# Optimization experiments

Measured on AMD Instinct MI355X. Metric: run time of the kernel, lower is better.

Reference implementation:

```python
import jax, jax.numpy as jnp
import numpy as np

N_NODES = 100000
N_EDGES = 10000
N_PAIRS = 1600000
F = 128


def setup_inputs() -> dict:
    key = jax.random.key(0)
    ks = jax.random.split(key, 7)
    x = jax.random.normal(ks[0], (N_NODES, F), dtype=jnp.float32)
    action = jax.random.uniform(ks[1], (N_NODES, 3), dtype=jnp.float32)
    W_msg = jax.random.normal(ks[2], (F, F), dtype=jnp.float32) * (1.0 / np.sqrt(F))
    W_upd = jax.random.normal(ks[3], (F, F), dtype=jnp.float32) * (1.0 / np.sqrt(F))
    b_upd = jax.random.normal(ks[4], (F,), dtype=jnp.float32) * 0.02
    pair_node = jax.random.randint(ks[5], (N_PAIRS,), 0, N_NODES, dtype=jnp.int32)
    pair_edge = jax.random.randint(ks[6], (N_PAIRS,), 0, N_EDGES, dtype=jnp.int32)
    return {"x": x, "action": action, "W_msg": W_msg, "W_upd": W_upd,
            "b_upd": b_upd, "pair_node": pair_node, "pair_edge": pair_edge}


def _v2v_mean(m, pair_node, pair_edge):
    # v2e: mean of incident node features per hyperedge, then
    # e2v: mean of incident hyperedge features per node.
    ones = jnp.ones((pair_node.shape[0],), dtype=m.dtype)
    edge_deg = jax.ops.segment_sum(ones, pair_edge, num_segments=N_EDGES)
    node_deg = jax.ops.segment_sum(ones, pair_node, num_segments=N_NODES)
    # gather node features to incidence pairs, reduce into edges  [E, F]
    e_feat = jax.ops.segment_sum(m[pair_node], pair_edge, num_segments=N_EDGES)
    e_feat = e_feat / jnp.maximum(edge_deg, 1.0)[:, None]
    # gather edge features back to pairs, reduce into nodes       [N, F]
    v_feat = jax.ops.segment_sum(e_feat[pair_edge], pair_node, num_segments=N_NODES)
    v_feat = v_feat / jnp.maximum(node_deg, 1.0)[:, None]
    return v_feat


def reference(x, action, W_msg, W_upd, b_upd, pair_node, pair_edge):
    send = action[:, 0] + action[:, 2]      # [N]
    receive = action[:, 0] + action[:, 1]   # [N]
    m_ji = x @ W_msg.T                       # lin_message (no bias)
    m_ji = jax.nn.gelu(m_ji, approximate=False)  # dropout=0 (eval)
    m_ji = m_ji * send[:, None]
    m_i = _v2v_mean(m_ji, pair_node, pair_edge)
    m_i = m_i * receive[:, None]
    h_i = jax.nn.gelu(x @ W_upd.T + b_upd + m_i, approximate=False)
    return h_i
```

## Files before the change

### kernel.cpp

```cpp
#include <hip/hip_runtime.h>

#define N_NODESC 100000
#define N_EDGESC 10000
#define N_PAIRSC 1600000
#define FDIM 128

#define NB 200
#define EPB 50
#define NPB 500
#define ECAP2 8704
#define PA_CHUNK 8192
#define PA_NCH ((N_PAIRSC + PA_CHUNK - 1) / PA_CHUNK)
#define MSG_BLKS 782

typedef short bf16x8 __attribute__((ext_vector_type(8)));
typedef float f32x4 __attribute__((ext_vector_type(4)));
typedef float f32x2 __attribute__((ext_vector_type(2)));
typedef int i32x4 __attribute__((ext_vector_type(4)));
typedef unsigned u32x4 __attribute__((ext_vector_type(4)));

__device__ __forceinline__ unsigned short f2b(float f) {
  unsigned u = __float_as_uint(f);
  u += 0x7fffu + ((u >> 16) & 1u);
  return (unsigned short)(u >> 16);
}
__device__ __forceinline__ float b2f(unsigned short b) {
  return __uint_as_float(((unsigned)b) << 16);
}
__device__ __forceinline__ unsigned pack2(float a, float b) {
  return (unsigned)f2b(a) | ((unsigned)f2b(b) << 16);
}
__device__ __forceinline__ float gelu_fast(float z) {
  float z2 = z * z;
  float w = fmaf(0.044715f, z2, 1.0f);
  float e = __expf(1.5957691216f * z * w);
  return z * e * __builtin_amdgcn_rcpf(e + 1.0f);
}
__device__ __forceinline__ bf16x8 ldA(const float* p) {
  float4 u0 = *(const float4*)p;
  float4 u1 = *(const float4*)(p + 4);
  u32x4 w = {pack2(u0.x, u0.y), pack2(u0.z, u0.w), pack2(u1.x, u1.y), pack2(u1.z, u1.w)};
  return __builtin_bit_cast(bf16x8, w);
}

__global__ __launch_bounds__(256) void k_prep(const float* __restrict__ action,
                                              const float* __restrict__ wmsg, const float* __restrict__ wupd,
                                              short* __restrict__ wmsgb, short* __restrict__ wupdb,
                                              float* __restrict__ send, float* __restrict__ recv,
                                              int* __restrict__ gcure, int* __restrict__ gcurn) {
  int i = blockIdx.x * 256 + threadIdx.x;
  if (i < FDIM * FDIM) {
    wmsgb[i] = (short)f2b(wmsg[i]);
    wupdb[i] = (short)f2b(wupd[i]);
  }
  if (i < N_NODESC) {
    float a0 = action[i * 3 + 0], a1 = action[i * 3 + 1], a2 = action[i * 3 + 2];
    send[i] = a0 + a2;
    recv[i] = a0 + a1;
  }
  if (i < NB) {
    gcure[i] = i * ECAP2;
    gcurn[i] = i * ECAP2;
  }
}

__device__ __forceinline__ int wave_incl_scan(int v, int lane) {
#pragma unroll
  for (int d = 1; d < 64; d <<= 1) {
    int n = __shfl_up(v, d, 64);
    if (lane >= d) v += n;
  }
  return v;
}

__global__ __launch_bounds__(256) void k_part_msg(const int* __restrict__ pn, const int* __restrict__ pe,
                                                  int* __restrict__ gcure, int* __restrict__ gcurn,
                                                  unsigned* __restrict__ buckE, unsigned* __restrict__ buckN,
                                                  const float* __restrict__ x, const short* __restrict__ wb,
                                                  const float* __restrict__ send,
                                                  unsigned char* __restrict__ mji8) {
  __shared__ unsigned stage[PA_CHUNK];
  __shared__ int ce[NB], cn[NB];
  int t = threadIdx.x;
  if (blockIdx.x < PA_NCH) {
    for (int i = t; i < NB; i += 256) { ce[i] = 0; cn[i] = 0; }
    __syncthreads();
    long long base = (long long)blockIdx.x * PA_CHUNK;
    for (int q = t; q < PA_CHUNK / 4; q += 256) {
      long long idx = base + (long long)q * 4;
      if (idx >= N_PAIRSC) break;
      i32x4 e4 = __builtin_nontemporal_load((const i32x4*)(pe + idx));
      i32x4 v4 = __builtin_nontemporal_load((const i32x4*)(pn + idx));
#pragma unroll
      for (int j = 0; j < 4; j++) {
        unsigned ee = (unsigned)e4[j], vv = (unsigned)v4[j];
        stage[q + j * (PA_CHUNK / 4)] = (ee << 17) | vv;
        atomicAdd(&ce[ee / EPB], 1);
        atomicAdd(&cn[vv / NPB], 1);
      }
    }
    __syncthreads();
    for (int i = t; i < NB; i += 256) {
      ce[i] = atomicAdd(&gcure[i], ce[i]);
      cn[i] = atomicAdd(&gcurn[i], cn[i]);
    }
    __syncthreads();
    for (int i = t; i < PA_CHUNK; i += 256) {
      int q = i & (PA_CHUNK / 4 - 1), j = i >> 11;
      long long idx = base + (long long)q * 4 + j;
      if (idx >= N_PAIRSC) continue;
      unsigned u = stage[i];
      unsigned ee = u >> 17, vv = u & 0x1FFFF;
      int p1 = atomicAdd(&ce[ee / EPB], 1);
      buckE[p1] = u;
      int p2 = atomicAdd(&cn[vv / NPB], 1);
      buckN[p2] = (vv << 14) | ee;
    }
  } else {
    int gw = ((int)(blockIdx.x - PA_NCH) * 256 + t) >> 6;
    int lane = t & 63;
    if (gw >= N_NODESC / 32) return;
    int rb = gw * 32;
    int lr = lane & 15, lg = lane >> 4;

    bf16x8 A0[4], A1[4];
    const float* xrow0 = x + (size_t)(rb + lr) * FDIM + lg * 8;
    const float* xrow1 = xrow0 + 16 * FDIM;
#pragma unroll
    for (int kk = 0; kk < 4; kk++) {
      A0[kk] = ldA(xrow0 + kk * 32);
      A1[kk] = ldA(xrow1 + kk * 32);
    }
    float sv0[4], sv1[4];
#pragma unroll
    for (int j = 0; j < 4; j++) {
      sv0[j] = send[rb + lg * 4 + j];
      sv1[j] = send[rb + 16 + lg * 4 + j];
    }
#pragma unroll
    for (int c = 0; c < 8; c++) {
      f32x4 acc0 = {0.f, 0.f, 0.f, 0.f}, acc1 = {0.f, 0.f, 0.f, 0.f};
      const short* wrow = wb + (size_t)(16 * c + lr) * FDIM + lg * 8;
#pragma unroll
      for (int kk = 0; kk < 4; kk++) {
        bf16x8 B = *(const bf16x8*)(wrow + kk * 32);
        acc0 = __builtin_amdgcn_mfma_f32_16x16x32_bf16(A0[kk], B, acc0, 0, 0, 0);
        acc1 = __builtin_amdgcn_mfma_f32_16x16x32_bf16(A1[kk], B, acc1, 0, 0, 0);
      }
      int col = 16 * c + lr;
#pragma unroll
      for (int j = 0; j < 4; j++) {
        float m0 = gelu_fast(acc0[j]) * sv0[j];
        float m1 = gelu_fast(acc1[j]) * sv1[j];
        int row0 = rb + lg * 4 + j;
        mji8[(size_t)row0 * FDIM + col] =
            (unsigned char)(__builtin_amdgcn_cvt_pk_fp8_f32(m0, m0, 0, false) & 0xFF);
        mji8[(size_t)(row0 + 16) * FDIM + col] =
            (unsigned char)(__builtin_amdgcn_cvt_pk_fp8_f32(m1, m1, 0, false) & 0xFF);
      }
    }
  }
}

__global__ __launch_bounds__(256) void k_fine_e(const unsigned* __restrict__ buckE,
                                                const int* __restrict__ gcure,
                                                int* __restrict__ ecnt, int* __restrict__ eoff,
                                                int* __restrict__ sn) {
  __shared__ int cnt_s[EPB], cur_s[EPB];
  int b = blockIdx.x, t = threadIdx.x;
  int lo = b * EPB, beg = b * ECAP2, end = gcure[b];
  if (t < EPB) cnt_s[t] = 0;
  __syncthreads();
  for (int i = beg + t; i < end; i += 256)
    atomicAdd(&cnt_s[(int)(buckE[i] >> 17) - lo], 1);
  __syncthreads();
  if (t < 64) {
    int v = (t < EPB) ? cnt_s[t] : 0;
    int inc = wave_incl_scan(v, t);
    if (t < EPB) cur_s[t] = beg + inc - v;
  }
  __syncthreads();
  if (t < EPB) {
    ecnt[lo + t] = cnt_s[t];
    eoff[lo + t] = cur_s[t];
  }
  __syncthreads();
  for (int i = beg + t; i < end; i += 256) {
    unsigned u = buckE[i];
    int key = (int)(u >> 17) - lo;
    int pos = atomicAdd(&cur_s[key], 1);
    sn[pos] = (int)(u & 0x1FFFF);
  }
}

__global__ __launch_bounds__(256) void k_edge_fineN(const unsigned* __restrict__ buckN,
                                                    const int* __restrict__ gcurn,
                                                    int* __restrict__ ncnt, int* __restrict__ noff,
                                                    int* __restrict__ se,
                                                    const unsigned char* __restrict__ mji8,
                                                    const int* __restrict__ sn,
                                                    const int* __restrict__ eoff, const int* __restrict__ ecnt,
                                                    unsigned char* __restrict__ efeat8) {
  __shared__ int cnt_s[NPB], cur_s[NPB];
  int t = threadIdx.x;
  if (blockIdx.x < NB) {
    int b = blockIdx.x;
    int lo = b * NPB, beg = b * ECAP2, end = gcurn[b];
    for (int i = t; i < NPB; i += 256) cnt_s[i] = 0;
    __syncthreads();
    for (int i = beg + t; i < end; i += 256)
      atomicAdd(&cnt_s[(int)(buckN[i] >> 14) - lo], 1);
    __syncthreads();
    if (t < 64) {
      int carry = beg;
#pragma unroll
      for (int base = 0; base < NPB; base += 64) {
        int idx = base + t;
        int v = (idx < NPB) ? cnt_s[idx] : 0;
        int inc = wave_incl_scan(v, t);
        if (idx < NPB) cur_s[idx] = carry + inc - v;
        carry += __shfl(inc, 63, 64);
      }
    }
    __syncthreads();
    for (int i = t; i < NPB; i += 256) {
      ncnt[lo + i] = cnt_s[i];
      noff[lo + i] = cur_s[i];
    }
    __syncthreads();
    for (int i = beg + t; i < end; i += 256) {
      unsigned u = buckN[i];
      int key = (int)(u >> 14) - lo;
      int pos = atomicAdd(&cur_s[key], 1);
      se[pos] = (int)(u & 0x3FFF);
    }
  } else {
    int wave = (int)(blockIdx.x - NB) * 4 + (t >> 6);
    int lane = t & 63;
    int half = lane >> 5, sub2 = (lane >> 4) & 1, c4 = lane & 15;
    int edge = wave * 2 + half;
    if (edge >= N_EDGESC) return;
    int beg = eoff[edge], cnt = ecnt[edge];
    f32x2 a0 = {0.f, 0.f}, a1 = {0.f, 0.f}, a2 = {0.f, 0.f}, a3 = {0.f, 0.f};
#pragma unroll 4
    for (int p = sub2; p < cnt; p += 2) {
      int node = sn[beg + p];
      uint2 u = ((const uint2*)(mji8 + (size_t)node * FDIM))[c4];
      a0 += __builtin_amdgcn_cvt_pk_f32_fp8(u.x, false);
      a1 += __builtin_amdgcn_cvt_pk_f32_fp8(u.x, true);
      a2 += __builtin_amdgcn_cvt_pk_f32_fp8(u.y, false);
      a3 += __builtin_amdgcn_cvt_pk_f32_fp8(u.y, true);
    }
    a0[0] += __shfl_xor(a0[0], 16, 64); a0[1] += __shfl_xor(a0[1], 16, 64);
    a1[0] += __shfl_xor(a1[0], 16, 64); a1[1] += __shfl_xor(a1[1], 16, 64);
    a2[0] += __shfl_xor(a2[0], 16, 64); a2[1] += __shfl_xor(a2[1], 16, 64);
    a3[0] += __shfl_xor(a3[0], 16, 64); a3[1] += __shfl_xor(a3[1], 16, 64);
    if (sub2 == 0) {
      float inv = 1.0f / fmaxf((float)cnt, 1.0f);
      uint2 o;
      o.x = (unsigned)__builtin_amdgcn_cvt_pk_fp8_f32(a0[0] * inv, a0[1] * inv, 0, false);
      o.x = (unsigned)__builtin_amdgcn_cvt_pk_fp8_f32(a1[0] * inv, a1[1] * inv, (int)o.x, true);
      o.y = (unsigned)__builtin_amdgcn_cvt_pk_fp8_f32(a2[0] * inv, a2[1] * inv, 0, false);
      o.y = (unsigned)__builtin_amdgcn_cvt_pk_fp8_f32(a3[0] * inv, a3[1] * inv, (int)o.y, true);
      ((uint2*)(efeat8 + (size_t)edge * FDIM))[c4] = o;
    }
  }
}

__global__ __launch_bounds__(256) void k_node(const unsigned char* __restrict__ efeat8, const int* __restrict__ se,
                                              const int* __restrict__ noff, const int* __restrict__ ncnt,
                                              const float* __restrict__ recv, unsigned char* __restrict__ mi8) {
  int wave = blockIdx.x * 4 + (threadIdx.x >> 6);
  int lane = threadIdx.x & 63;
  int sub = lane >> 4, c4 = lane & 15;
  int node = wave * 4 + sub;
  int beg = noff[node], cnt = ncnt[node];
  f32x2 a0 = {0.f, 0.f}, a1 = {0.f, 0.f}, a2 = {0.f, 0.f}, a3 = {0.f, 0.f};
#pragma unroll 4
  for (int p = 0; p < cnt; p++) {
    int e = se[beg + p];
    uint2 u = ((const uint2*)(efeat8 + (size_t)e * FDIM))[c4];
    a0 += __builtin_amdgcn_cvt_pk_f32_fp8(u.x, false);
    a1 += __builtin_amdgcn_cvt_pk_f32_fp8(u.x, true);
    a2 += __builtin_amdgcn_cvt_pk_f32_fp8(u.y, false);
    a3 += __builtin_amdgcn_cvt_pk_f32_fp8(u.y, true);
  }
  float s = recv[node] / fmaxf((float)cnt, 1.0f);
  uint2 o;
  o.x = (unsigned)__builtin_amdgcn_cvt_pk_fp8_f32(a0[0] * s, a0[1] * s, 0, false);
  o.x = (unsigned)__builtin_amdgcn_cvt_pk_fp8_f32(a1[0] * s, a1[1] * s, (int)o.x, true);
  o.y = (unsigned)__builtin_amdgcn_cvt_pk_fp8_f32(a2[0] * s, a2[1] * s, 0, false);
  o.y = (unsigned)__builtin_amdgcn_cvt_pk_fp8_f32(a3[0] * s, a3[1] * s, (int)o.y, true);
  ((uint2*)(mi8 + (size_t)node * FDIM))[c4] = o;
}

__global__ __launch_bounds__(256) void k_gemm_upd(const float* __restrict__ x, const short* __restrict__ wb,
                                                  const float* __restrict__ bias,
                                                  const unsigned char* __restrict__ mi8,
                                                  float* __restrict__ out) {
  int gw = (blockIdx.x * 256 + threadIdx.x) >> 6;
  int lane = threadIdx.x & 63;
  if (gw >= N_NODESC / 32) return;
  int rb = gw * 32;
  int lr = lane & 15, lg = lane >> 4;

  bf16x8 A0[4], A1[4];
  const float* xrow0 = x + (size_t)(rb + lr) * FDIM + lg * 8;
  const float* xrow1 = xrow0 + 16 * FDIM;
#pragma unroll
  for (int kk = 0; kk < 4; kk++) {
    A0[kk] = ldA(xrow0 + kk * 32);
    A1[kk] = ldA(xrow1 + kk * 32);
  }

#pragma unroll
  for (int c = 0; c < 8; c++) {
    f32x4 acc0 = {0.f, 0.f, 0.f, 0.f}, acc1 = {0.f, 0.f, 0.f, 0.f};
    const short* wrow = wb + (size_t)(16 * c + lr) * FDIM + lg * 8;
#pragma unroll
    for (int kk = 0; kk < 4; kk++) {
      bf16x8 B = *(const bf16x8*)(wrow + kk * 32);
      acc0 = __builtin_amdgcn_mfma_f32_16x16x32_bf16(A0[kk], B, acc0, 0, 0, 0);
      acc1 = __builtin_amdgcn_mfma_f32_16x16x32_bf16(A1[kk], B, acc1, 0, 0, 0);
    }
    int col = 16 * c + lr;
    float bc = bias[col];
#pragma unroll
    for (int j = 0; j < 4; j++) {
      int row0 = rb + lg * 4 + j;
      f32x2 m0 = __builtin_amdgcn_cvt_pk_f32_fp8((unsigned)mi8[(size_t)row0 * FDIM + col], false);
      f32x2 m1 = __builtin_amdgcn_cvt_pk_f32_fp8((unsigned)mi8[(size_t)(row0 + 16) * FDIM + col], false);
      float z0 = acc0[j] + bc + m0[0];
      float z1 = acc1[j] + bc + m1[0];
      __builtin_nontemporal_store(gelu_fast(z0), &out[(size_t)row0 * FDIM + col]);
      __builtin_nontemporal_store(gelu_fast(z1), &out[(size_t)(row0 + 16) * FDIM + col]);
    }
  }
}

extern "C" void kernel_launch(void* const* d_in, const int* in_sizes, int n_in,
                              void* d_out, int out_size, void* d_ws, size_t ws_size,
                              hipStream_t stream) {
  const float* x = (const float*)d_in[0];
  const float* action = (const float*)d_in[1];
  const float* wmsg = (const float*)d_in[2];
  const float* wupd = (const float*)d_in[3];
  const float* bupd = (const float*)d_in[4];
  const int* pn = (const int*)d_in[5];
  const int* pe = (const int*)d_in[6];
  float* out = (float*)d_out;

  char* p = (char*)d_ws;
  auto alloc = [&](size_t bytes) -> char* {
    char* r = p;
    p += (bytes + 255) & ~(size_t)255;
    return r;
  };
  unsigned char* mji8 = (unsigned char*)alloc((size_t)N_NODESC * FDIM);
  unsigned char* mi8 = (unsigned char*)alloc((size_t)N_NODESC * FDIM);
  unsigned char* efeat8 = (unsigned char*)alloc((size_t)N_EDGESC * FDIM);
  unsigned* buckE = (unsigned*)alloc((size_t)NB * ECAP2 * 4);
  unsigned* buckN = (unsigned*)alloc((size_t)NB * ECAP2 * 4);
  int* sn = (int*)alloc((size_t)NB * ECAP2 * 4);
  int* se = (int*)alloc((size_t)NB * ECAP2 * 4);
  short* wmsgb = (short*)alloc(FDIM * FDIM * 2);
  short* wupdb = (short*)alloc(FDIM * FDIM * 2);
  float* send = (float*)alloc(N_NODESC * 4);
  float* recv = (float*)alloc(N_NODESC * 4);
  int* ecnt = (int*)alloc(N_EDGESC * 4);
  int* eoff = (int*)alloc(N_EDGESC * 4);
  int* ncnt = (int*)alloc(N_NODESC * 4);
  int* noff = (int*)alloc(N_NODESC * 4);
  int* gcure = (int*)alloc(NB * 4);
  int* gcurn = (int*)alloc(NB * 4);

  k_prep<<<391, 256, 0, stream>>>(action, wmsg, wupd, wmsgb, wupdb, send, recv, gcure, gcurn);
  k_part_msg<<<PA_NCH + MSG_BLKS, 256, 0, stream>>>(pn, pe, gcure, gcurn, buckE, buckN,
                                                    x, wmsgb, send, mji8);
  k_fine_e<<<NB, 256, 0, stream>>>(buckE, gcure, ecnt, eoff, sn);
  k_edge_fineN<<<NB + 1250, 256, 0, stream>>>(buckN, gcurn, ncnt, noff, se,
                                              mji8, sn, eoff, ecnt, efeat8);
  k_node<<<6250, 256, 0, stream>>>(efeat8, se, noff, ncnt, recv, mi8);
  k_gemm_upd<<<782, 256, 0, stream>>>(x, wupdb, bupd, mi8, out);
}
```

Before: 164.7 us.

## Locally sort partition chunks in LDS so bucket scatters write contiguously

```diff
diff --git a/kernel.cpp b/kernel.cpp
--- a/kernel.cpp
+++ b/kernel.cpp
@@ -9,7 +9,7 @@
 #define EPB 50
 #define NPB 500
 #define ECAP2 8704
-#define PA_CHUNK 8192
+#define PA_CHUNK 6144
 #define PA_NCH ((N_PAIRSC + PA_CHUNK - 1) / PA_CHUNK)
 #define MSG_BLKS 782
 
@@ -80,12 +80,14 @@
                                                   const float* __restrict__ send,
                                                   unsigned char* __restrict__ mji8) {
   __shared__ unsigned stage[PA_CHUNK];
-  __shared__ int ce[NB], cn[NB];
+  __shared__ unsigned ordered[PA_CHUNK];
+  __shared__ int ce[NB], cn[NB], lsE[NB], lsN[NB], curE[NB], curN[NB], gbE[NB], gbN[NB];
   int t = threadIdx.x;
   if (blockIdx.x < PA_NCH) {
     for (int i = t; i < NB; i += 256) { ce[i] = 0; cn[i] = 0; }
     __syncthreads();
     long long base = (long long)blockIdx.x * PA_CHUNK;
+    int nItems = (int)(((long long)N_PAIRSC - base) < PA_CHUNK ? (N_PAIRSC - base) : PA_CHUNK);
     for (int q = t; q < PA_CHUNK / 4; q += 256) {
       long long idx = base + (long long)q * 4;
       if (idx >= N_PAIRSC) break;
@@ -94,27 +96,61 @@
 #pragma unroll
       for (int j = 0; j < 4; j++) {
         unsigned ee = (unsigned)e4[j], vv = (unsigned)v4[j];
-        stage[q + j * (PA_CHUNK / 4)] = (ee << 17) | vv;
+        stage[q * 4 + j] = (ee << 17) | vv;
         atomicAdd(&ce[ee / EPB], 1);
         atomicAdd(&cn[vv / NPB], 1);
       }
     }
     __syncthreads();
-    for (int i = t; i < NB; i += 256) {
-      ce[i] = atomicAdd(&gcure[i], ce[i]);
-      cn[i] = atomicAdd(&gcurn[i], cn[i]);
-    }
-    __syncthreads();
-    for (int i = t; i < PA_CHUNK; i += 256) {
-      int q = i & (PA_CHUNK / 4 - 1), j = i >> 11;
-      long long idx = base + (long long)q * 4 + j;
-      if (idx >= N_PAIRSC) continue;
+    if (t < 64) {
+      int carry = 0;
+      for (int b0 = 0; b0 < NB; b0 += 64) {
+        int idx = b0 + t;
+        int v = (idx < NB) ? ce[idx] : 0;
+        int inc = wave_incl_scan(v, t);
+        if (idx < NB) lsE[idx] = carry + inc - v;
+        carry += __shfl(inc, 63, 64);
+      }
+    } else if (t < 128) {
+      int lane = t - 64;
+      int carry = 0;
+      for (int b0 = 0; b0 < NB; b0 += 64) {
+        int idx = b0 + lane;
+        int v = (idx < NB) ? cn[idx] : 0;
+        int inc = wave_incl_scan(v, lane);
+        if (idx < NB) lsN[idx] = carry + inc - v;
+        carry += __shfl(inc, 63, 64);
+      }
+    }
+    __syncthreads();
+    if (t < NB) {
+      gbE[t] = atomicAdd(&gcure[t], ce[t]);
+      gbN[t] = atomicAdd(&gcurn[t], cn[t]);
+      curE[t] = lsE[t];
+      curN[t] = lsN[t];
+    }
+    __syncthreads();
+    for (int i = t; i < nItems; i += 256) {
       unsigned u = stage[i];
+      int b = (int)(u >> 17) / EPB;
+      int pos = atomicAdd(&curE[b], 1);
+      ordered[pos] = u;
+    }
+    __syncthreads();
+    for (int i = t; i < nItems; i += 256) {
+      unsigned u = ordered[i];
       unsigned ee = u >> 17, vv = u & 0x1FFFF;
-      int p1 = atomicAdd(&ce[ee / EPB], 1);
-      buckE[p1] = u;
-      int p2 = atomicAdd(&cn[vv / NPB], 1);
-      buckN[p2] = (vv << 14) | ee;
+      int be = (int)ee / EPB;
+      buckE[gbE[be] + (i - lsE[be])] = u;
+      int bn = (int)vv / NPB;
+      int pos = atomicAdd(&curN[bn], 1);
+      stage[pos] = (vv << 14) | ee;
+    }
+    __syncthreads();
+    for (int i = t; i < nItems; i += 256) {
+      unsigned u = stage[i];
+      int bn = (int)(u >> 14) / NPB;
+      buckN[gbN[bn] + (i - lsN[bn])] = u;
     }
   } else {
     int gw = ((int)(blockIdx.x - PA_NCH) * 256 + t) >> 6;
```

Result: faster. 160.3 us (-2.7%).

## Split pair partitioning per key and locally sort before coalesced bucket writes

Applied to the files above, without the earlier changes.

```diff
diff --git a/kernel.cpp b/kernel.cpp
--- a/kernel.cpp
+++ b/kernel.cpp
@@ -79,13 +79,45 @@
                                                   const float* __restrict__ x, const short* __restrict__ wb,
                                                   const float* __restrict__ send,
                                                   unsigned char* __restrict__ mji8) {
-  __shared__ unsigned stage[PA_CHUNK];
-  __shared__ int ce[NB], cn[NB];
+  __shared__ unsigned ordered[PA_CHUNK];
+  __shared__ int cb[NB], ls[NB], cur[NB], gb[NB];
   int t = threadIdx.x;
-  if (blockIdx.x < PA_NCH) {
-    for (int i = t; i < NB; i += 256) { ce[i] = 0; cn[i] = 0; }
-    __syncthreads();
-    long long base = (long long)blockIdx.x * PA_CHUNK;
+  if (blockIdx.x < 2 * PA_NCH) {
+    int isN = blockIdx.x >= PA_NCH;
+    int blk = isN ? (int)blockIdx.x - PA_NCH : (int)blockIdx.x;
+    int* gcur = isN ? gcurn : gcure;
+    unsigned* buck = isN ? buckN : buckE;
+    long long base = (long long)blk * PA_CHUNK;
+    int nItems = (int)(((long long)N_PAIRSC - base) < PA_CHUNK ? (N_PAIRSC - base) : PA_CHUNK);
+    for (int i = t; i < NB; i += 256) cb[i] = 0;
+    __syncthreads();
+    for (int q = t; q < PA_CHUNK / 4; q += 256) {
+      long long idx = base + (long long)q * 4;
+      if (idx >= N_PAIRSC) break;
+      i32x4 k4 = __builtin_nontemporal_load((const i32x4*)((isN ? pn : pe) + idx));
+#pragma unroll
+      for (int j = 0; j < 4; j++) {
+        int b = isN ? (k4[j] / NPB) : (k4[j] / EPB);
+        atomicAdd(&cb[b], 1);
+      }
+    }
+    __syncthreads();
+    if (t < 64) {
+      int carry = 0;
+      for (int b0 = 0; b0 < NB; b0 += 64) {
+        int idx = b0 + t;
+        int v = (idx < NB) ? cb[idx] : 0;
+        int inc = wave_incl_scan(v, t);
+        if (idx < NB) ls[idx] = carry + inc - v;
+        carry += __shfl(inc, 63, 64);
+      }
+    }
+    __syncthreads();
+    if (t < NB) {
+      gb[t] = atomicAdd(&gcur[t], cb[t]);
+      cur[t] = ls[t];
+    }
+    __syncthreads();
     for (int q = t; q < PA_CHUNK / 4; q += 256) {
       long long idx = base + (long long)q * 4;
       if (idx >= N_PAIRSC) break;
@@ -94,30 +126,21 @@
 #pragma unroll
       for (int j = 0; j < 4; j++) {
         unsigned ee = (unsigned)e4[j], vv = (unsigned)v4[j];
-        stage[q + j * (PA_CHUNK / 4)] = (ee << 17) | vv;
-        atomicAdd(&ce[ee / EPB], 1);
-        atomicAdd(&cn[vv / NPB], 1);
-      }
-    }
-    __syncthreads();
-    for (int i = t; i < NB; i += 256) {
-      ce[i] = atomicAdd(&gcure[i], ce[i]);
-      cn[i] = atomicAdd(&gcurn[i], cn[i]);
-    }
-    __syncthreads();
-    for (int i = t; i < PA_CHUNK; i += 256) {
-      int q = i & (PA_CHUNK / 4 - 1), j = i >> 11;
-      long long idx = base + (long long)q * 4 + j;
-      if (idx >= N_PAIRSC) continue;
-      unsigned u = stage[i];
-      unsigned ee = u >> 17, vv = u & 0x1FFFF;
-      int p1 = atomicAdd(&ce[ee / EPB], 1);
-      buckE[p1] = u;
-      int p2 = atomicAdd(&cn[vv / NPB], 1);
-      buckN[p2] = (vv << 14) | ee;
+        unsigned u = isN ? ((vv << 14) | ee) : ((ee << 17) | vv);
+        int b = isN ? (int)(vv / NPB) : (int)(ee / EPB);
+        int pos = atomicAdd(&cur[b], 1);
+        ordered[pos] = u;
+      }
+    }
+    __syncthreads();
+    int shift = isN ? 14 : 17;
+    for (int i = t; i < nItems; i += 256) {
+      unsigned u = ordered[i];
+      int b = isN ? (int)((u >> shift) / NPB) : (int)((u >> shift) / EPB);
+      buck[gb[b] + (i - ls[b])] = u;
     }
   } else {
-    int gw = ((int)(blockIdx.x - PA_NCH) * 256 + t) >> 6;
+    int gw = ((int)(blockIdx.x - 2 * PA_NCH) * 256 + t) >> 6;
     int lane = t & 63;
     if (gw >= N_NODESC / 32) return;
     int rb = gw * 32;
@@ -375,8 +398,8 @@
   int* gcurn = (int*)alloc(NB * 4);
 
   k_prep<<<391, 256, 0, stream>>>(action, wmsg, wupd, wmsgb, wupdb, send, recv, gcure, gcurn);
-  k_part_msg<<<PA_NCH + MSG_BLKS, 256, 0, stream>>>(pn, pe, gcure, gcurn, buckE, buckN,
-                                                    x, wmsgb, send, mji8);
+  k_part_msg<<<2 * PA_NCH + MSG_BLKS, 256, 0, stream>>>(pn, pe, gcure, gcurn, buckE, buckN,
+                                                        x, wmsgb, send, mji8);
   k_fine_e<<<NB, 256, 0, stream>>>(buckE, gcure, ecnt, eoff, sn);
   k_edge_fineN<<<NB + 1250, 256, 0, stream>>>(buckN, gcurn, ncnt, noff, se,
                                               mji8, sn, eoff, ecnt, efeat8);
```

New measurement: 158.9 us (median of 2 runs). -3.5%, faster.
